# Kernel optimization log

Hardware: AMD Instinct MI355X
Metric: run time of the kernel (lower is better)

The kernel has to match this reference:

```python
import jax, jax.numpy as jnp
import numpy as np

B, N, CIN, COUT = 2, 150000, 64, 64
SPATIAL = (128, 128, 128)  # spatial_shape forward arg, fixed here (list arg)
EPS = 1e-5


def setup_inputs() -> dict:
    key = jax.random.key(0)
    k1, k2, k3 = jax.random.split(key, 3)
    features = jax.random.normal(k1, (B, N, CIN), jnp.float32)
    coordinates = jax.random.randint(k2, (B, N, 3), 0, SPATIAL[0], jnp.int32)
    # SparseConv3d weight: 3x3x3 kernel flattened to 27 offsets, [27, Cin, Cout]
    weight = jax.random.normal(k3, (27, CIN, COUT), jnp.float32) * 0.05
    gamma = jnp.ones((COUT,), jnp.float32)
    beta = jnp.zeros((COUT,), jnp.float32)
    return {"features": features, "coordinates": coordinates, "weight": weight,
            "gamma": gamma, "beta": beta, "batch_size": B}


def _rulebook_ids(coordinates, batch_size):
    """For each of 27 kernel offsets, the flat input-point id feeding each output
    site (output sites = input sites, rulebook gather). Empty/OOB -> BN (zero row)."""
    X, Y, Z = SPATIAL
    Np = coordinates.shape[1]
    BN = batch_size * Np
    pid = jnp.arange(BN, dtype=jnp.int32)
    b = jnp.repeat(jnp.arange(batch_size, dtype=jnp.int32), Np)
    c = coordinates.reshape(-1, 3)
    # dense voxel hash: coord -> point id (max for deterministic collision handling)
    grid = jnp.full((batch_size, X, Y, Z), -1, jnp.int32)
    grid = grid.at[b, c[:, 0], c[:, 1], c[:, 2]].max(pid)
    # 27 offsets in {-1,0,1}^3 (padding=1, kernel=3, stride=1)
    r = jnp.arange(-1, 2, dtype=jnp.int32)
    offs = jnp.stack(jnp.meshgrid(r, r, r, indexing="ij"), -1).reshape(27, 3)
    nc = c[None, :, :] + offs[:, None, :]                      # [27, BN, 3]
    hi = jnp.array([X, Y, Z], jnp.int32)
    valid = jnp.all((nc >= 0) & (nc < hi), axis=-1)            # [27, BN]
    ncc = jnp.clip(nc, 0, hi - 1)
    ids = grid[b[None, :], ncc[..., 0], ncc[..., 1], ncc[..., 2]]
    return jnp.where(valid & (ids >= 0), ids, BN)              # BN -> zero row


def reference(features, coordinates, weight, gamma, beta, batch_size):
    Bs, Np, Cin = features.shape
    BN = Bs * Np
    ids = _rulebook_ids(coordinates, batch_size)               # [27, BN]
    feats = jnp.concatenate(
        [features.reshape(BN, Cin), jnp.zeros((1, Cin), features.dtype)], 0)

    # gather-GEMM-scatter accumulated over the 27 kernel offsets
    def step(acc, xs):
        idk, wk = xs
        return acc + feats[idk] @ wk, None

    out0 = jnp.zeros((BN, weight.shape[-1]), features.dtype)
    out, _ = jax.lax.scan(step, out0, (ids, weight))

    # BatchNorm1d (training stats over all points) + ReLU
    mean = out.mean(axis=0)
    var = out.var(axis=0)
    out = (out - mean) * jax.lax.rsqrt(var + EPS) * gamma + beta
    out = jax.nn.relu(out)
    return out.reshape(Bs, Np, -1)
```

## Files before the change

kernel.cpp:

```cpp
#include <hip/hip_runtime.h>

#define GS 128
#define GS3 (GS*GS*GS)
#define NPTS 150000
#define NBATCH 2
#define BN_TOT (NBATCH*NPTS)
#define CONV_BLOCKS 2344
#define BN_PAD (CONV_BLOCKS*128)
#define ZROW   BN_PAD
#define EPS 1e-5f
#define NBKT 8192

#define OFF_GRID   0ull
#define SZ_GRID    ((size_t)NBATCH*GS3*4)
#define OFF_WFRAG  (OFF_GRID + SZ_GRID)
#define SZ_WFRAG   ((size_t)27*4096*2)
#define OFF_STATS  (OFF_WFRAG + SZ_WFRAG)
#define OFF_CNT    (OFF_STATS + 512)
#define OFF_CUR    (OFF_CNT + NBKT*4)
#define OFF_SIDX   (OFF_CUR + NBKT*4)
#define OFF_CSORT  (OFF_SIDX + 1200128)
#define OFF_FB16S  (OFF_CSORT + (size_t)BN_PAD*16)
#define OFF_IDS    (OFF_FB16S + (size_t)(BN_PAD+1)*128)

typedef __attribute__((ext_vector_type(8))) short bf16x8;
typedef __attribute__((ext_vector_type(4))) float f32x4;
typedef unsigned int u32;
typedef const __attribute__((address_space(1))) u32* gas_u32p;
typedef __attribute__((address_space(3))) u32* las_u32p;

__device__ __forceinline__ short f2bf(float f) {
    union { float f; unsigned u; } v; v.f = f;
    unsigned rr = v.u + 0x7fffu + ((v.u >> 16) & 1u);
    return (short)(rr >> 16);
}

__global__ __launch_bounds__(256) void k_count(const int* __restrict__ coords,
                                               int* __restrict__ grid,
                                               u32* __restrict__ cnt) {
    int p = blockIdx.x*256 + threadIdx.x;
    if (p >= BN_TOT) return;
    int x = coords[p*3+0], y = coords[p*3+1], z = coords[p*3+2];
    int b = (p >= NPTS);
    atomicMax(&grid[(b<<21) | (x<<14) | (y<<7) | z], p);
    atomicAdd(&cnt[(b<<12) | ((x>>3)<<8) | ((y>>3)<<4) | (z>>3)], 1u);
}

__global__ __launch_bounds__(1024) void k_scan(const u32* __restrict__ cnt,
                                               u32* __restrict__ cur) {
    __shared__ u32 ps[1024];
    int t = threadIdx.x;
    u32 l[8]; u32 s = 0;
    #pragma unroll
    for (int i = 0; i < 8; ++i) { l[i] = cnt[t*8+i]; s += l[i]; }
    ps[t] = s; __syncthreads();
    for (int off = 1; off < 1024; off <<= 1) {
        u32 v = (t >= off) ? ps[t-off] : 0u; __syncthreads();
        ps[t] += v; __syncthreads();
    }
    u32 run = (t == 0) ? 0u : ps[t-1];
    #pragma unroll
    for (int i = 0; i < 8; ++i) { cur[t*8+i] = run; run += l[i]; }
}

__global__ __launch_bounds__(256) void k_place(const float* __restrict__ feats,
                                               const int* __restrict__ coords,
                                               u32* __restrict__ cur,
                                               int* __restrict__ sortidx,
                                               int4* __restrict__ csorted,
                                               ushort* __restrict__ fb16s) {
    int p = blockIdx.x*256 + threadIdx.x;
    if (p >= BN_PAD) return;
    if (p >= BN_TOT) { csorted[p] = make_int4(-9,-9,-9,0); return; }
    int x = coords[p*3+0], y = coords[p*3+1], z = coords[p*3+2];
    int b = (p >= NPTS);
    int bkt = (b<<12) | ((x>>3)<<8) | ((y>>3)<<4) | (z>>3);
    int pos = (int)atomicAdd(&cur[bkt], 1u);
    sortidx[p] = pos;
    csorted[pos] = make_int4(x, y, z, p);
    const float4* s = (const float4*)(feats + (size_t)p*64);
    ushort* d = fb16s + (size_t)pos*64;
    #pragma unroll
    for (int i = 0; i < 8; ++i) {
        float4 a = s[2*i], c = s[2*i+1];
        ushort4 u0 = { (ushort)f2bf(a.x),(ushort)f2bf(a.y),(ushort)f2bf(a.z),(ushort)f2bf(a.w) };
        ushort4 u1 = { (ushort)f2bf(c.x),(ushort)f2bf(c.y),(ushort)f2bf(c.z),(ushort)f2bf(c.w) };
        ((ushort4*)d)[2*i] = u0; ((ushort4*)d)[2*i+1] = u1;
    }
}

__global__ __launch_bounds__(256) void k_ids(const int4* __restrict__ csorted,
                                             const int* __restrict__ grid,
                                             const int* __restrict__ sortidx,
                                             int* __restrict__ ids) {
    int s = blockIdx.x*256 + threadIdx.x;
    if (s >= BN_PAD) return;
    int4 c = csorted[s];
    const bool pad = (s >= BN_TOT);
    const int gb = (c.w >= NPTS) ? GS3 : 0;
    #pragma unroll
    for (int k = 0; k < 27; ++k) {
        int dx = k/9 - 1, dy = (k/3)%3 - 1, dz = k%3 - 1;
        int nx = c.x+dx, ny = c.y+dy, nz = c.z+dz;
        int sid = ZROW;
        if (!pad && (((unsigned)nx < 128u) & ((unsigned)ny < 128u) &
                     ((unsigned)nz < 128u))) {
            int pid = grid[gb + (nx<<14) + (ny<<7) + nz];
            if (pid >= 0) sid = sortidx[pid];
        }
        ids[(size_t)k*BN_PAD + s] = sid;
    }
}

__global__ __launch_bounds__(256) void k_prefrag(const float* __restrict__ w,
                                                 short* __restrict__ wfrag) {
    int t = blockIdx.x * 256 + threadIdx.x;
    if (t >= 27*2*4*64*8) return;
    int i    = t & 7;
    int lane = (t >> 3) & 63;
    int tt   = (t >> 9) & 3;
    int c    = (t >> 11) & 1;
    int k    = t >> 12;
    int kk = c*32 + (lane >> 4)*8 + i;
    int co = tt*16 + (lane & 15);
    wfrag[t] = f2bf(w[(k*64 + kk)*64 + co]);
}

__global__ __launch_bounds__(256, 3) void k_conv(
    const ushort* __restrict__ fb16s,
    const int4* __restrict__ csorted,
    const int* __restrict__ ids_g,
    const ushort* __restrict__ wfrag,
    float* __restrict__ out,
    float* __restrict__ gstats)
{
    __shared__ __align__(16) ushort ldsB[2][4096];
    __shared__ int ids_lds[27*128];
    __shared__ float bsum[64], bsq[64];

    const int tid  = threadIdx.x;
    const int lane = tid & 63;
    const int wv   = tid >> 6;
    const int r    = lane & 15;
    const int seg  = lane >> 4;
    const int p0b  = blockIdx.x * 128;
    const int wrow = wv*32 + r;

    auto stage = [&](int kk, int bsel) {
        const u32* g = (const u32*)(wfrag + (size_t)kk*4096) + tid*4;
        u32* l  = (u32*)(&ldsB[bsel][wv*512]);
        __builtin_amdgcn_global_load_lds((gas_u32p)g,  (las_u32p)l,  16, 0, 0);
        const u32* g2 = g + 1024;
        u32* l2 = (u32*)(&ldsB[bsel][2048 + wv*512]);
        __builtin_amdgcn_global_load_lds((gas_u32p)g2, (las_u32p)l2, 16, 0, 0);
    };

#define LDA4(AC, sid0, sid1) {                                            \
        const ushort* a0_ = fb16s + (size_t)(sid0)*64 + seg*8;            \
        const ushort* a1_ = fb16s + (size_t)(sid1)*64 + seg*8;            \
        AC[0] = *(const bf16x8*)(a0_);  AC[1] = *(const bf16x8*)(a0_+32); \
        AC[2] = *(const bf16x8*)(a1_);  AC[3] = *(const bf16x8*)(a1_+32); }

    f32x4 t0q0={0,0,0,0}, t0q1={0,0,0,0}, t0q2={0,0,0,0}, t0q3={0,0,0,0};
    f32x4 t1q0={0,0,0,0}, t1q1={0,0,0,0}, t1q2={0,0,0,0}, t1q3={0,0,0,0};
    bf16x8 aE[4], aO[4];

    #pragma unroll
    for (int c = 0; c < 14; ++c) {
        int idx = c*256 + tid;
        if (idx < 27*128)
            ids_lds[idx] = ids_g[(size_t)(idx>>7)*BN_PAD + p0b + (idx&127)];
    }
    int i00 = ids_g[p0b + wrow];
    int i01 = ids_g[p0b + wrow + 16];
    int i10 = ids_g[(size_t)BN_PAD + p0b + wrow];
    int i11 = ids_g[(size_t)BN_PAD + p0b + wrow + 16];
    __syncthreads();
    __builtin_amdgcn_sched_barrier(0);
    LDA4(aE, i00, i01);
    __builtin_amdgcn_sched_barrier(0);
    stage(0, 0);
    __builtin_amdgcn_sched_barrier(0);
    LDA4(aO, i10, i11);
    __builtin_amdgcn_sched_barrier(0);

    auto phase = [&](int k, bf16x8 (&AC)[4], int bsel) {
        asm volatile("s_waitcnt vmcnt(4)" ::: "memory");
        __builtin_amdgcn_sched_barrier(0);
        __builtin_amdgcn_s_barrier();
        __builtin_amdgcn_sched_barrier(0);
        const bf16x8* bb = (const bf16x8*)ldsB[bsel];
        bf16x8 b0 = bb[0*64+lane], b1 = bb[1*64+lane],
               b2 = bb[2*64+lane], b3 = bb[3*64+lane],
               b4 = bb[4*64+lane], b5 = bb[5*64+lane],
               b6 = bb[6*64+lane], b7 = bb[7*64+lane];
        int kp2 = (k+2 > 26) ? 26 : k+2;
        int idn0 = ids_lds[kp2*128 + wrow];
        int idn1 = ids_lds[kp2*128 + wrow + 16];
        if (k < 26) stage(k+1, bsel^1);
        __builtin_amdgcn_sched_barrier(0);
        t0q0 = __builtin_amdgcn_mfma_f32_16x16x32_bf16(AC[0], b0, t0q0, 0,0,0);
        t0q1 = __builtin_amdgcn_mfma_f32_16x16x32_bf16(AC[0], b1, t0q1, 0,0,0);
        t0q2 = __builtin_amdgcn_mfma_f32_16x16x32_bf16(AC[0], b2, t0q2, 0,0,0);
        t0q3 = __builtin_amdgcn_mfma_f32_16x16x32_bf16(AC[0], b3, t0q3, 0,0,0);
        t0q0 = __builtin_amdgcn_mfma_f32_16x16x32_bf16(AC[1], b4, t0q0, 0,0,0);
        t0q1 = __builtin_amdgcn_mfma_f32_16x16x32_bf16(AC[1], b5, t0q1, 0,0,0);
        t0q2 = __builtin_amdgcn_mfma_f32_16x16x32_bf16(AC[1], b6, t0q2, 0,0,0);
        t0q3 = __builtin_amdgcn_mfma_f32_16x16x32_bf16(AC[1], b7, t0q3, 0,0,0);
        t1q0 = __builtin_amdgcn_mfma_f32_16x16x32_bf16(AC[2], b0, t1q0, 0,0,0);
        t1q1 = __builtin_amdgcn_mfma_f32_16x16x32_bf16(AC[2], b1, t1q1, 0,0,0);
        t1q2 = __builtin_amdgcn_mfma_f32_16x16x32_bf16(AC[2], b2, t1q2, 0,0,0);
        t1q3 = __builtin_amdgcn_mfma_f32_16x16x32_bf16(AC[2], b3, t1q3, 0,0,0);
        t1q0 = __builtin_amdgcn_mfma_f32_16x16x32_bf16(AC[3], b4, t1q0, 0,0,0);
        t1q1 = __builtin_amdgcn_mfma_f32_16x16x32_bf16(AC[3], b5, t1q1, 0,0,0);
        t1q2 = __builtin_amdgcn_mfma_f32_16x16x32_bf16(AC[3], b6, t1q2, 0,0,0);
        t1q3 = __builtin_amdgcn_mfma_f32_16x16x32_bf16(AC[3], b7, t1q3, 0,0,0);
        __builtin_amdgcn_sched_barrier(0);
        if (k < 26) { LDA4(AC, idn0, idn1); }
        __builtin_amdgcn_sched_barrier(0);
    };

    #pragma unroll 1
    for (int t = 0; t < 13; ++t) {
        phase(2*t,   aE, 0);
        phase(2*t+1, aO, 1);
    }
    phase(26, aE, 0);

    #pragma unroll
    for (int j = 0; j < 4; ++j) {
        int row0 = p0b + wv*32 + seg*4 + j;
        if (row0 < BN_TOT) {
            int opid = csorted[row0].w;
            float* ob = out + (size_t)opid*64 + r;
            ob[ 0] = t0q0[j]; ob[16] = t0q1[j]; ob[32] = t0q2[j]; ob[48] = t0q3[j];
        }
        int row1 = row0 + 16;
        if (row1 < BN_TOT) {
            int opid = csorted[row1].w;
            float* ob = out + (size_t)opid*64 + r;
            ob[ 0] = t1q0[j]; ob[16] = t1q1[j]; ob[32] = t1q2[j]; ob[48] = t1q3[j];
        }
    }

    if (tid < 64) { bsum[tid] = 0.f; bsq[tid] = 0.f; }
    __syncthreads();
    float s0=0,s1=0,s2=0,s3=0,q0=0,q1=0,q2=0,q3=0;
    #pragma unroll
    for (int j = 0; j < 4; ++j) {
        s0 += t0q0[j] + t1q0[j];  q0 += t0q0[j]*t0q0[j] + t1q0[j]*t1q0[j];
        s1 += t0q1[j] + t1q1[j];  q1 += t0q1[j]*t0q1[j] + t1q1[j]*t1q1[j];
        s2 += t0q2[j] + t1q2[j];  q2 += t0q2[j]*t0q2[j] + t1q2[j]*t1q2[j];
        s3 += t0q3[j] + t1q3[j];  q3 += t0q3[j]*t0q3[j] + t1q3[j]*t1q3[j];
    }
    atomicAdd(&bsum[ 0 + r], s0);  atomicAdd(&bsq[ 0 + r], q0);
    atomicAdd(&bsum[16 + r], s1);  atomicAdd(&bsq[16 + r], q1);
    atomicAdd(&bsum[32 + r], s2);  atomicAdd(&bsq[32 + r], q2);
    atomicAdd(&bsum[48 + r], s3);  atomicAdd(&bsq[48 + r], q3);
    __syncthreads();
    if (tid < 64) { atomicAdd(&gstats[tid], bsum[tid]); atomicAdd(&gstats[64+tid], bsq[tid]); }
#undef LDA4
}

__global__ __launch_bounds__(256) void k_norm(float* __restrict__ out,
                                              const float* __restrict__ stats,
                                              const float* __restrict__ gamma,
                                              const float* __restrict__ beta) {
    int i = blockIdx.x*256 + threadIdx.x;
    const int n4 = BN_TOT*16;
    if (i >= n4) return;
    float4 v = ((const float4*)out)[i];
    int ch = (i & 15) * 4;
    float o[4] = {v.x, v.y, v.z, v.w};
    float rp[4];
    #pragma unroll
    for (int j = 0; j < 4; ++j) {
        int c = ch + j;
        float mean = stats[c] * (1.f/BN_TOT);
        float var  = stats[64+c] * (1.f/BN_TOT) - mean*mean;
        float y = (o[j] - mean) * rsqrtf(var + EPS) * gamma[c] + beta[c];
        rp[j] = fmaxf(y, 0.f);
    }
    float4 rv; rv.x = rp[0]; rv.y = rp[1]; rv.z = rp[2]; rv.w = rp[3];
    ((float4*)out)[i] = rv;
}

extern "C" void kernel_launch(void* const* d_in, const int* in_sizes, int n_in,
                              void* d_out, int out_size, void* d_ws, size_t ws_size,
                              hipStream_t stream) {
    const float* feats  = (const float*)d_in[0];
    const int*   coords = (const int*)d_in[1];
    const float* weight = (const float*)d_in[2];
    const float* gamma  = (const float*)d_in[3];
    const float* beta   = (const float*)d_in[4];
    float* out = (float*)d_out;

    char*   ws      = (char*)d_ws;
    int*    grid    = (int*)(ws + OFF_GRID);
    short*  wfrag   = (short*)(ws + OFF_WFRAG);
    float*  stats   = (float*)(ws + OFF_STATS);
    u32*    cnt     = (u32*)(ws + OFF_CNT);
    u32*    cur     = (u32*)(ws + OFF_CUR);
    int*    sortidx = (int*)(ws + OFF_SIDX);
    int4*   csorted = (int4*)(ws + OFF_CSORT);
    ushort* fb16s   = (ushort*)(ws + OFF_FB16S);
    int*    idbuf   = (int*)(ws + OFF_IDS);

    hipMemsetAsync(grid,  0xFF, SZ_GRID, stream);
    hipMemsetAsync(stats, 0, 512, stream);
    hipMemsetAsync(cnt,   0, NBKT*4, stream);
    hipMemsetAsync(fb16s + (size_t)BN_TOT*64, 0,
                   (size_t)(BN_PAD + 1 - BN_TOT)*128, stream);

    k_count  <<<(BN_TOT + 255)/256, 256, 0, stream>>>(coords, grid, cnt);
    k_scan   <<<1, 1024, 0, stream>>>(cnt, cur);
    k_place  <<<(BN_PAD + 255)/256, 256, 0, stream>>>(feats, coords, cur,
                                                      sortidx, csorted, fb16s);
    k_ids    <<<(BN_PAD + 255)/256, 256, 0, stream>>>(csorted, grid, sortidx, idbuf);
    k_prefrag<<<(27*2*4*64*8)/256, 256, 0, stream>>>(weight, wfrag);
    k_conv   <<<CONV_BLOCKS, 256, 0, stream>>>(fb16s, csorted, idbuf,
                                               (const ushort*)wfrag, out, stats);
    k_norm   <<<(BN_TOT*16)/256, 256, 0, stream>>>(out, stats, gamma, beta);
}
```

Before: 270.4 us.

## Fuse rulebook id computation into conv kernel and double rows per block

Removes the separate k_ids kernel and its 27xBN id buffer. Each conv block now computes its own neighbor ids from the voxel grid straight into LDS. The conv tile grows from 128 to 256 rows per block (64 rows per wave), so each weight stage is reused across more rows, at the cost of more registers and lower occupancy (launch bounds 2). MFMA issue is wrapped in setprio. The fused hash lookups add latency at block start that is not hidden by the pipeline.

```diff
diff --git a/kernel.cpp b/kernel.cpp
--- a/kernel.cpp
+++ b/kernel.cpp
@@ -5,8 +5,8 @@
 #define NPTS 150000
 #define NBATCH 2
 #define BN_TOT (NBATCH*NPTS)
-#define CONV_BLOCKS 2344
-#define BN_PAD (CONV_BLOCKS*128)
+#define CONV_BLOCKS 1172
+#define BN_PAD (CONV_BLOCKS*256)
 #define ZROW   BN_PAD
 #define EPS 1e-5f
 #define NBKT 8192
@@ -21,7 +21,6 @@
 #define OFF_SIDX   (OFF_CUR + NBKT*4)
 #define OFF_CSORT  (OFF_SIDX + 1200128)
 #define OFF_FB16S  (OFF_CSORT + (size_t)BN_PAD*16)
-#define OFF_IDS    (OFF_FB16S + (size_t)(BN_PAD+1)*128)
 
 typedef __attribute__((ext_vector_type(8))) short bf16x8;
 typedef __attribute__((ext_vector_type(4))) float f32x4;
@@ -89,33 +88,10 @@
     }
 }
 
-__global__ __launch_bounds__(256) void k_ids(const int4* __restrict__ csorted,
-                                             const int* __restrict__ grid,
-                                             const int* __restrict__ sortidx,
-                                             int* __restrict__ ids) {
-    int s = blockIdx.x*256 + threadIdx.x;
-    if (s >= BN_PAD) return;
-    int4 c = csorted[s];
-    const bool pad = (s >= BN_TOT);
-    const int gb = (c.w >= NPTS) ? GS3 : 0;
-    #pragma unroll
-    for (int k = 0; k < 27; ++k) {
-        int dx = k/9 - 1, dy = (k/3)%3 - 1, dz = k%3 - 1;
-        int nx = c.x+dx, ny = c.y+dy, nz = c.z+dz;
-        int sid = ZROW;
-        if (!pad && (((unsigned)nx < 128u) & ((unsigned)ny < 128u) &
-                     ((unsigned)nz < 128u))) {
-            int pid = grid[gb + (nx<<14) + (ny<<7) + nz];
-            if (pid >= 0) sid = sortidx[pid];
-        }
-        ids[(size_t)k*BN_PAD + s] = sid;
-    }
-}
-
 __global__ __launch_bounds__(256) void k_prefrag(const float* __restrict__ w,
                                                  short* __restrict__ wfrag) {
     int t = blockIdx.x * 256 + threadIdx.x;
-    if (t >= 27*2*4*64*8) return;
+    if (t >= 27*4096) return;
     int i    = t & 7;
     int lane = (t >> 3) & 63;
     int tt   = (t >> 9) & 3;
@@ -126,16 +102,17 @@
     wfrag[t] = f2bf(w[(k*64 + kk)*64 + co]);
 }
 
-__global__ __launch_bounds__(256, 3) void k_conv(
+__global__ __launch_bounds__(256, 2) void k_conv(
     const ushort* __restrict__ fb16s,
     const int4* __restrict__ csorted,
-    const int* __restrict__ ids_g,
+    const int* __restrict__ grid,
+    const int* __restrict__ sortidx,
     const ushort* __restrict__ wfrag,
     float* __restrict__ out,
     float* __restrict__ gstats)
 {
-    __shared__ __align__(16) ushort ldsB[2][4096];
-    __shared__ int ids_lds[27*128];
+    __shared__ __align__(16) ushort bufs[2][4096];
+    __shared__ int ids_lds[27*256];
     __shared__ float bsum[64], bsq[64];
 
     const int tid  = threadIdx.x;
@@ -143,123 +120,140 @@
     const int wv   = tid >> 6;
     const int r    = lane & 15;
     const int seg  = lane >> 4;
-    const int p0b  = blockIdx.x * 128;
-    const int wrow = wv*32 + r;
+    const int p0b  = blockIdx.x * 256;
+    const int rbase = wv*64 + r;
+
+    {
+        int4 c = csorted[p0b + tid];
+        const bool pad = (p0b + tid >= BN_TOT);
+        const int gb = (c.w >= NPTS) ? GS3 : 0;
+        #pragma unroll
+        for (int k = 0; k < 27; ++k) {
+            int dx = k/9 - 1, dy = (k/3)%3 - 1, dz = k%3 - 1;
+            int nx = c.x+dx, ny = c.y+dy, nz = c.z+dz;
+            int ok = (int)(!pad & ((unsigned)nx < 128u) & ((unsigned)ny < 128u) &
+                           ((unsigned)nz < 128u));
+            int pid = grid[gb + ((nx&127)<<14) + ((ny&127)<<7) + (nz&127)];
+            pid = ok ? pid : -1;
+            int sv = sortidx[pid < 0 ? 0 : pid];
+            ids_lds[k*256 + tid] = (pid >= 0) ? sv : ZROW;
+        }
+    }
+    if (tid < 64) { bsum[tid] = 0.f; bsq[tid] = 0.f; }
+    __syncthreads();
 
     auto stage = [&](int kk, int bsel) {
-        const u32* g = (const u32*)(wfrag + (size_t)kk*4096) + tid*4;
-        u32* l  = (u32*)(&ldsB[bsel][wv*512]);
-        __builtin_amdgcn_global_load_lds((gas_u32p)g,  (las_u32p)l,  16, 0, 0);
-        const u32* g2 = g + 1024;
-        u32* l2 = (u32*)(&ldsB[bsel][2048 + wv*512]);
-        __builtin_amdgcn_global_load_lds((gas_u32p)g2, (las_u32p)l2, 16, 0, 0);
+        #pragma unroll
+        for (int c = 0; c < 2; ++c) {
+            int chunk = c*4 + wv;
+            const u32* g = (const u32*)(wfrag + (size_t)kk*4096 + chunk*512) + lane*4;
+            u32* l = (u32*)(&bufs[bsel][chunk*512]);
+            __builtin_amdgcn_global_load_lds((gas_u32p)g, (las_u32p)l, 16, 0, 0);
+        }
     };
 
-#define LDA4(AC, sid0, sid1) {                                            \
-        const ushort* a0_ = fb16s + (size_t)(sid0)*64 + seg*8;            \
-        const ushort* a1_ = fb16s + (size_t)(sid1)*64 + seg*8;            \
-        AC[0] = *(const bf16x8*)(a0_);  AC[1] = *(const bf16x8*)(a0_+32); \
-        AC[2] = *(const bf16x8*)(a1_);  AC[3] = *(const bf16x8*)(a1_+32); }
-
-    f32x4 t0q0={0,0,0,0}, t0q1={0,0,0,0}, t0q2={0,0,0,0}, t0q3={0,0,0,0};
-    f32x4 t1q0={0,0,0,0}, t1q1={0,0,0,0}, t1q2={0,0,0,0}, t1q3={0,0,0,0};
-    bf16x8 aE[4], aO[4];
-
-    #pragma unroll
-    for (int c = 0; c < 14; ++c) {
-        int idx = c*256 + tid;
-        if (idx < 27*128)
-            ids_lds[idx] = ids_g[(size_t)(idx>>7)*BN_PAD + p0b + (idx&127)];
-    }
-    int i00 = ids_g[p0b + wrow];
-    int i01 = ids_g[p0b + wrow + 16];
-    int i10 = ids_g[(size_t)BN_PAD + p0b + wrow];
-    int i11 = ids_g[(size_t)BN_PAD + p0b + wrow + 16];
-    __syncthreads();
+#define LDA16(AC, S) { _Pragma("unroll") for (int t_ = 0; t_ < 4; ++t_) {     \
+        const ushort* ap_ = fb16s + (size_t)(S)[t_]*64 + seg*8;               \
+        AC[2*t_]   = *(const bf16x8*)(ap_);                                   \
+        AC[2*t_+1] = *(const bf16x8*)(ap_ + 32); } }
+#define LDIDS(S, kk) { _Pragma("unroll") for (int t_ = 0; t_ < 4; ++t_)       \
+        S[t_] = ids_lds[(kk)*256 + rbase + t_*16]; }
+
+    f32x4 acc[4][4];
+    #pragma unroll
+    for (int t = 0; t < 4; ++t)
+        #pragma unroll
+        for (int q = 0; q < 4; ++q) acc[t][q] = (f32x4){0,0,0,0};
+
+    bf16x8 aE[8], aO[8];
+    int sE[4], sO[4];
+
+    LDIDS(sE, 0); LDIDS(sO, 1);
     __builtin_amdgcn_sched_barrier(0);
-    LDA4(aE, i00, i01);
+    LDA16(aE, sE);
     __builtin_amdgcn_sched_barrier(0);
     stage(0, 0);
     __builtin_amdgcn_sched_barrier(0);
-    LDA4(aO, i10, i11);
+    LDA16(aO, sO);
     __builtin_amdgcn_sched_barrier(0);
 
-    auto phase = [&](int k, bf16x8 (&AC)[4], int bsel) {
-        asm volatile("s_waitcnt vmcnt(4)" ::: "memory");
+    auto phase = [&](int k, bf16x8 (&AC)[8]) {
+        asm volatile("s_waitcnt vmcnt(8)" ::: "memory");
         __builtin_amdgcn_sched_barrier(0);
         __builtin_amdgcn_s_barrier();
         __builtin_amdgcn_sched_barrier(0);
-        const bf16x8* bb = (const bf16x8*)ldsB[bsel];
-        bf16x8 b0 = bb[0*64+lane], b1 = bb[1*64+lane],
-               b2 = bb[2*64+lane], b3 = bb[3*64+lane],
-               b4 = bb[4*64+lane], b5 = bb[5*64+lane],
-               b6 = bb[6*64+lane], b7 = bb[7*64+lane];
+        const ushort* bb = bufs[k & 1];
+        bf16x8 b0 = *(const bf16x8*)(bb + 0*512 + lane*8);
+        bf16x8 b1 = *(const bf16x8*)(bb + 1*512 + lane*8);
+        bf16x8 b2 = *(const bf16x8*)(bb + 2*512 + lane*8);
+        bf16x8 b3 = *(const bf16x8*)(bb + 3*512 + lane*8);
+        bf16x8 b4 = *(const bf16x8*)(bb + 4*512 + lane*8);
+        bf16x8 b5 = *(const bf16x8*)(bb + 5*512 + lane*8);
+        bf16x8 b6 = *(const bf16x8*)(bb + 6*512 + lane*8);
+        bf16x8 b7 = *(const bf16x8*)(bb + 7*512 + lane*8);
         int kp2 = (k+2 > 26) ? 26 : k+2;
-        int idn0 = ids_lds[kp2*128 + wrow];
-        int idn1 = ids_lds[kp2*128 + wrow + 16];
-        if (k < 26) stage(k+1, bsel^1);
-        __builtin_amdgcn_sched_barrier(0);
-        t0q0 = __builtin_amdgcn_mfma_f32_16x16x32_bf16(AC[0], b0, t0q0, 0,0,0);
-        t0q1 = __builtin_amdgcn_mfma_f32_16x16x32_bf16(AC[0], b1, t0q1, 0,0,0);
-        t0q2 = __builtin_amdgcn_mfma_f32_16x16x32_bf16(AC[0], b2, t0q2, 0,0,0);
-        t0q3 = __builtin_amdgcn_mfma_f32_16x16x32_bf16(AC[0], b3, t0q3, 0,0,0);
-        t0q0 = __builtin_amdgcn_mfma_f32_16x16x32_bf16(AC[1], b4, t0q0, 0,0,0);
-        t0q1 = __builtin_amdgcn_mfma_f32_16x16x32_bf16(AC[1], b5, t0q1, 0,0,0);
-        t0q2 = __builtin_amdgcn_mfma_f32_16x16x32_bf16(AC[1], b6, t0q2, 0,0,0);
-        t0q3 = __builtin_amdgcn_mfma_f32_16x16x32_bf16(AC[1], b7, t0q3, 0,0,0);
-        t1q0 = __builtin_amdgcn_mfma_f32_16x16x32_bf16(AC[2], b0, t1q0, 0,0,0);
-        t1q1 = __builtin_amdgcn_mfma_f32_16x16x32_bf16(AC[2], b1, t1q1, 0,0,0);
-        t1q2 = __builtin_amdgcn_mfma_f32_16x16x32_bf16(AC[2], b2, t1q2, 0,0,0);
-        t1q3 = __builtin_amdgcn_mfma_f32_16x16x32_bf16(AC[2], b3, t1q3, 0,0,0);
-        t1q0 = __builtin_amdgcn_mfma_f32_16x16x32_bf16(AC[3], b4, t1q0, 0,0,0);
-        t1q1 = __builtin_amdgcn_mfma_f32_16x16x32_bf16(AC[3], b5, t1q1, 0,0,0);
-        t1q2 = __builtin_amdgcn_mfma_f32_16x16x32_bf16(AC[3], b6, t1q2, 0,0,0);
-        t1q3 = __builtin_amdgcn_mfma_f32_16x16x32_bf16(AC[3], b7, t1q3, 0,0,0);
-        __builtin_amdgcn_sched_barrier(0);
-        if (k < 26) { LDA4(AC, idn0, idn1); }
+        int sn[4]; LDIDS(sn, kp2);
+        if (k < 26) stage(k+1, (k+1) & 1);
+        __builtin_amdgcn_sched_barrier(0);
+        __builtin_amdgcn_s_setprio(1);
+        #pragma unroll
+        for (int t = 0; t < 4; ++t) {
+            acc[t][0] = __builtin_amdgcn_mfma_f32_16x16x32_bf16(AC[2*t], b0, acc[t][0], 0,0,0);
+            acc[t][1] = __builtin_amdgcn_mfma_f32_16x16x32_bf16(AC[2*t], b1, acc[t][1], 0,0,0);
+            acc[t][2] = __builtin_amdgcn_mfma_f32_16x16x32_bf16(AC[2*t], b2, acc[t][2], 0,0,0);
+            acc[t][3] = __builtin_amdgcn_mfma_f32_16x16x32_bf16(AC[2*t], b3, acc[t][3], 0,0,0);
+            acc[t][0] = __builtin_amdgcn_mfma_f32_16x16x32_bf16(AC[2*t+1], b4, acc[t][0], 0,0,0);
+            acc[t][1] = __builtin_amdgcn_mfma_f32_16x16x32_bf16(AC[2*t+1], b5, acc[t][1], 0,0,0);
+            acc[t][2] = __builtin_amdgcn_mfma_f32_16x16x32_bf16(AC[2*t+1], b6, acc[t][2], 0,0,0);
+            acc[t][3] = __builtin_amdgcn_mfma_f32_16x16x32_bf16(AC[2*t+1], b7, acc[t][3], 0,0,0);
+        }
+        __builtin_amdgcn_s_setprio(0);
+        __builtin_amdgcn_sched_barrier(0);
+        LDA16(AC, sn);
         __builtin_amdgcn_sched_barrier(0);
     };
 
     #pragma unroll 1
     for (int t = 0; t < 13; ++t) {
-        phase(2*t,   aE, 0);
-        phase(2*t+1, aO, 1);
-    }
-    phase(26, aE, 0);
-
-    #pragma unroll
-    for (int j = 0; j < 4; ++j) {
-        int row0 = p0b + wv*32 + seg*4 + j;
-        if (row0 < BN_TOT) {
-            int opid = csorted[row0].w;
-            float* ob = out + (size_t)opid*64 + r;
-            ob[ 0] = t0q0[j]; ob[16] = t0q1[j]; ob[32] = t0q2[j]; ob[48] = t0q3[j];
+        phase(2*t,   aE);
+        phase(2*t+1, aO);
+    }
+    phase(26, aE);
+
+    #pragma unroll
+    for (int t = 0; t < 4; ++t) {
+        #pragma unroll
+        for (int j = 0; j < 4; ++j) {
+            int row = p0b + wv*64 + t*16 + seg*4 + j;
+            if (row < BN_TOT) {
+                int opid = csorted[row].w;
+                float* ob = out + (size_t)opid*64 + r;
+                ob[ 0] = acc[t][0][j];
+                ob[16] = acc[t][1][j];
+                ob[32] = acc[t][2][j];
+                ob[48] = acc[t][3][j];
+            }
         }
-        int row1 = row0 + 16;
-        if (row1 < BN_TOT) {
-            int opid = csorted[row1].w;
-            float* ob = out + (size_t)opid*64 + r;
-            ob[ 0] = t1q0[j]; ob[16] = t1q1[j]; ob[32] = t1q2[j]; ob[48] = t1q3[j];
-        }
-    }
-
-    if (tid < 64) { bsum[tid] = 0.f; bsq[tid] = 0.f; }
-    __syncthreads();
-    float s0=0,s1=0,s2=0,s3=0,q0=0,q1=0,q2=0,q3=0;
-    #pragma unroll
-    for (int j = 0; j < 4; ++j) {
-        s0 += t0q0[j] + t1q0[j];  q0 += t0q0[j]*t0q0[j] + t1q0[j]*t1q0[j];
-        s1 += t0q1[j] + t1q1[j];  q1 += t0q1[j]*t0q1[j] + t1q1[j]*t1q1[j];
-        s2 += t0q2[j] + t1q2[j];  q2 += t0q2[j]*t0q2[j] + t1q2[j]*t1q2[j];
-        s3 += t0q3[j] + t1q3[j];  q3 += t0q3[j]*t0q3[j] + t1q3[j]*t1q3[j];
-    }
-    atomicAdd(&bsum[ 0 + r], s0);  atomicAdd(&bsq[ 0 + r], q0);
-    atomicAdd(&bsum[16 + r], s1);  atomicAdd(&bsq[16 + r], q1);
-    atomicAdd(&bsum[32 + r], s2);  atomicAdd(&bsq[32 + r], q2);
-    atomicAdd(&bsum[48 + r], s3);  atomicAdd(&bsq[48 + r], q3);
+    }
+
+    float s_[4] = {0,0,0,0}, q_[4] = {0,0,0,0};
+    #pragma unroll
+    for (int q = 0; q < 4; ++q)
+        #pragma unroll
+        for (int t = 0; t < 4; ++t)
+            #pragma unroll
+            for (int j = 0; j < 4; ++j) {
+                float v = acc[t][q][j]; s_[q] += v; q_[q] += v*v;
+            }
+    #pragma unroll
+    for (int q = 0; q < 4; ++q) {
+        atomicAdd(&bsum[q*16 + r], s_[q]);
+        atomicAdd(&bsq [q*16 + r], q_[q]);
+    }
     __syncthreads();
     if (tid < 64) { atomicAdd(&gstats[tid], bsum[tid]); atomicAdd(&gstats[64+tid], bsq[tid]); }
-#undef LDA4
+#undef LDA16
+#undef LDIDS
 }
 
 __global__ __launch_bounds__(256) void k_norm(float* __restrict__ out,
@@ -304,7 +298,6 @@
     int*    sortidx = (int*)(ws + OFF_SIDX);
     int4*   csorted = (int4*)(ws + OFF_CSORT);
     ushort* fb16s   = (ushort*)(ws + OFF_FB16S);
-    int*    idbuf   = (int*)(ws + OFF_IDS);
 
     hipMemsetAsync(grid,  0xFF, SZ_GRID, stream);
     hipMemsetAsync(stats, 0, 512, stream);
@@ -316,9 +309,8 @@
     k_scan   <<<1, 1024, 0, stream>>>(cnt, cur);
     k_place  <<<(BN_PAD + 255)/256, 256, 0, stream>>>(feats, coords, cur,
                                                       sortidx, csorted, fb16s);
-    k_ids    <<<(BN_PAD + 255)/256, 256, 0, stream>>>(csorted, grid, sortidx, idbuf);
-    k_prefrag<<<(27*2*4*64*8)/256, 256, 0, stream>>>(weight, wfrag);
-    k_conv   <<<CONV_BLOCKS, 256, 0, stream>>>(fb16s, csorted, idbuf,
+    k_prefrag<<<(27*4096)/256, 256, 0, stream>>>(weight, wfrag);
+    k_conv   <<<CONV_BLOCKS, 256, 0, stream>>>(fb16s, csorted, grid, sortidx,
                                                (const ushort*)wfrag, out, stats);
     k_norm   <<<(BN_TOT*16)/256, 256, 0, stream>>>(out, stats, gamma, beta);
 }
```

Result: faster. 227.0 us (-16.0%).
